# Performance work log

Measured on AMD Instinct MI355X. Metric: run time of the kernel, lower is better.

## Reference

```python
import jax, jax.numpy as jnp
import numpy as np

N = 50000   # nodes
E = 1600000 # edges (before self loops)
G = 512     # graphs in the batch
NEG = 0.2   # GATv2 leaky_relu negative slope


def _seg_softmax(s, seg, n):
    m = jax.ops.segment_max(s, seg, num_segments=n)
    e = jnp.exp(s - m[seg])
    z = jax.ops.segment_sum(e, seg, num_segments=n)
    return e / z[seg]


def _gatv2(x, src, dst, ea, Wl, bl, Wr, br, We, att, bias, n):
    # PyG GATv2Conv, heads=1: e_ij = att . leaky_relu(Wl x_j + Wr x_i + We e_ij)
    xl = x @ Wl + bl
    xr = x @ Wr + br
    h = jax.nn.leaky_relu(xl[src] + xr[dst] + ea @ We, NEG)  # [E+N, C]
    alpha = _seg_softmax(h @ att, dst, n)                    # softmax over dst neighborhoods
    return jax.ops.segment_sum(alpha[:, None] * xl[src], dst, num_segments=n) + bias


def _add_self_loops(src, dst, ea, n):
    # fill_value='mean': self-loop edge_attr = mean of incoming edge_attr (0 if none)
    deg = jax.ops.segment_sum(jnp.ones_like(dst, dtype=ea.dtype), dst, num_segments=n)
    loop = jax.ops.segment_sum(ea, dst, num_segments=n) / jnp.maximum(deg, 1.0)[:, None]
    ar = jnp.arange(n, dtype=src.dtype)
    return (jnp.concatenate([src, ar]), jnp.concatenate([dst, ar]),
            jnp.concatenate([ea, loop], axis=0))


def _glorot(key, fan_in, fan_out):
    return jax.random.normal(key, (fan_in, fan_out), dtype=jnp.float32) / np.sqrt(fan_in)


def setup_inputs() -> dict:
    key = jax.random.key(0)
    ks = jax.random.split(key, 20)
    x = jax.random.normal(ks[0], (N, 16), dtype=jnp.float32)
    edge_index = jax.random.randint(ks[1], (2, E), 0, N, dtype=jnp.int32)
    edge_attr = jax.random.normal(ks[2], (E, 18), dtype=jnp.float32)
    batch_ids = jnp.sort(jax.random.randint(ks[3], (N,), 0, G, dtype=jnp.int32))
    z = lambda c: jnp.zeros((c,), dtype=jnp.float32)
    return {
        'x': x, 'edge_index': edge_index, 'edge_attr': edge_attr, 'batch_ids': batch_ids,
        # GATv2Conv(16, 100, edge_dim=18)
        'W1l': _glorot(ks[4], 16, 100), 'b1l': z(100),
        'W1r': _glorot(ks[5], 16, 100), 'b1r': z(100),
        'W1e': _glorot(ks[6], 18, 100),
        'a1': jax.random.normal(ks[7], (100,), dtype=jnp.float32) * 0.1, 'c1': z(100),
        # GATv2Conv(100, 200, edge_dim=18)
        'W2l': _glorot(ks[8], 100, 200), 'b2l': z(200),
        'W2r': _glorot(ks[9], 100, 200), 'b2r': z(200),
        'W2e': _glorot(ks[10], 18, 200),
        'a2': jax.random.normal(ks[11], (200,), dtype=jnp.float32) * 0.1, 'c2': z(200),
        # Linear(200, 400)
        'W3': _glorot(ks[12], 200, 400), 'b3': z(400),
        # FFN 400->200->100->100
        'F1': _glorot(ks[13], 400, 200), 'bf1': z(200),
        'F2': _glorot(ks[14], 200, 100), 'bf2': z(100),
        'F3': _glorot(ks[15], 100, 100), 'bf3': z(100),
    }


def reference(x, edge_index, edge_attr, batch_ids,
              W1l, b1l, W1r, b1r, W1e, a1, c1,
              W2l, b2l, W2r, b2r, W2e, a2, c2,
              W3, b3, F1, bf1, F2, bf2, F3, bf3):
    src, dst, ea = _add_self_loops(edge_index[0], edge_index[1], edge_attr, N)
    h = jax.nn.relu(_gatv2(x, src, dst, ea, W1l, b1l, W1r, b1r, W1e, a1, c1, N))
    h = jax.nn.relu(_gatv2(h, src, dst, ea, W2l, b2l, W2r, b2r, W2e, a2, c2, N))
    h = h @ W3 + b3  # [N, 400]
    cnt = jax.ops.segment_sum(jnp.ones((N,), dtype=h.dtype), batch_ids, num_segments=G)
    pooled = jax.ops.segment_sum(h, batch_ids, num_segments=G) / jnp.maximum(cnt, 1.0)[:, None]
    y = jax.nn.relu(pooled @ F1 + bf1)
    y = jax.nn.relu(y @ F2 + bf2)
    return y @ F3 + bf3  # [G, 100]
```

## Files before the change

### kernel.cpp

```cpp
#include <hip/hip_runtime.h>
#include <cstdint>
#include <climits>
#include <math.h>

#define NN 50000
#define EE 1600000
#define ET (EE + NN)
#define GG 512
#define NEG_SLOPE 0.2f
#define NB 196

typedef _Float16 half2v __attribute__((ext_vector_type(2)));

__device__ __forceinline__ uint32_t packh2(float a, float b) {
    union { half2v h; uint32_t u; } c;
    c.h = half2v{(_Float16)a, (_Float16)b};
    return c.u;
}
__device__ __forceinline__ float2 uph(uint32_t u) {
    union { uint32_t u; half2v h; } c;
    c.u = u;
    return make_float2((float)c.h.x, (float)c.h.y);
}
__device__ __forceinline__ float fdot2u(uint32_t a, uint32_t b, float c) {
    union { uint32_t u; half2v h; } ua, ub;
    ua.u = a; ub.u = b;
    return __builtin_amdgcn_fdot2(ua.h, ub.h, c, false);
}
__device__ __forceinline__ float rlanef(float v, int l) {
    return __int_as_float(__builtin_amdgcn_readlane(__float_as_int(v), l));
}

__global__ void k_hist(const int* __restrict__ dst, int* __restrict__ hist) {
    int e = blockIdx.x * blockDim.x + threadIdx.x;
    if (e < EE) atomicAdd(&hist[dst[e]], 1);
}

__global__ void k_scan_a(const int* __restrict__ hist, int* __restrict__ bsum) {
    __shared__ int tmp[256];
    int i = blockIdx.x * 256 + threadIdx.x;
    tmp[threadIdx.x] = (i < NN) ? hist[i] : 0;
    __syncthreads();
    for (int d = 128; d; d >>= 1) {
        if (threadIdx.x < d) tmp[threadIdx.x] += tmp[threadIdx.x + d];
        __syncthreads();
    }
    if (threadIdx.x == 0) bsum[blockIdx.x] = tmp[0];
}

__global__ void k_scan_b(int* __restrict__ bsum, int* __restrict__ rowptr) {
    __shared__ int tmp[256];
    int t = threadIdx.x;
    int v = (t < NB) ? bsum[t] : 0;
    tmp[t] = v;
    __syncthreads();
    for (int d = 1; d < 256; d <<= 1) {
        int u = (t >= d) ? tmp[t - d] : 0;
        __syncthreads();
        tmp[t] += u;
        __syncthreads();
    }
    if (t < NB) bsum[t] = tmp[t] - v;
    if (t == 255) rowptr[NN] = tmp[255];
}

__global__ void k_scan_c(const int* __restrict__ hist, const int* __restrict__ bsum,
                         int* __restrict__ rowptr, int* __restrict__ cursor) {
    __shared__ int tmp[256];
    int i = blockIdx.x * 256 + threadIdx.x;
    int v = (i < NN) ? hist[i] : 0;
    tmp[threadIdx.x] = v;
    __syncthreads();
    for (int d = 1; d < 256; d <<= 1) {
        int t = (threadIdx.x >= d) ? tmp[threadIdx.x - d] : 0;
        __syncthreads();
        tmp[threadIdx.x] += t;
        __syncthreads();
    }
    if (i < NN) {
        int rp = tmp[threadIdx.x] - v + bsum[blockIdx.x];
        rowptr[i] = rp;
        cursor[i] = rp;
    }
}

__global__ void k_scatter(const int* __restrict__ srcv, const int* __restrict__ dstv,
                          const float* __restrict__ ea, int* __restrict__ cursor,
                          int* __restrict__ csr_src, int* __restrict__ csr_dst,
                          uint32_t* __restrict__ eaa) {
    int e = blockIdx.x * blockDim.x + threadIdx.x;
    if (e >= EE) return;
    int d = dstv[e];
    int p = atomicAdd(&cursor[d], 1);
    csr_src[p] = srcv[e];
    csr_dst[p] = d;
    const float* r = ea + (size_t)e * 18;
    uint32_t o[12];
#pragma unroll
    for (int kk = 0; kk < 9; kk++) {
        float2 q = *(const float2*)(r + 2 * kk);
        o[kk] = packh2(q.x, q.y);
    }
    o[9] = o[10] = o[11] = 0;
    uint4* dst = (uint4*)(eaa + (size_t)p * 12);
    dst[0] = *(uint4*)&o[0];
    dst[1] = *(uint4*)&o[4];
    dst[2] = *(uint4*)&o[8];
}

__global__ void __launch_bounds__(256)
k_loop2(const int* __restrict__ rowptr, uint32_t* __restrict__ eaa,
        int* __restrict__ csr_src, int* __restrict__ csr_dst) {
    const int lane = threadIdx.x & 63;
    int wid = blockIdx.x * (blockDim.x >> 6) + (threadIdx.x >> 6);
    int nw = gridDim.x * (blockDim.x >> 6);

    for (int i = wid; i < NN; i += nw) {
        int beg = __builtin_amdgcn_readfirstlane(rowptr[i]);
        int end = __builtin_amdgcn_readfirstlane(rowptr[i + 1]);
        float s[18];
#pragma unroll
        for (int j = 0; j < 18; j++) s[j] = 0.f;
        for (int cs = beg; cs < end; cs += 64) {
            int cnt = end - cs; if (cnt > 64) cnt = 64;
            if (lane < cnt) {
                const uint32_t* pe = eaa + (size_t)(cs + lane) * 12;
                uint4 a = *(const uint4*)pe;
                uint4 b = *(const uint4*)(pe + 4);
                uint32_t c = pe[8];
                uint32_t w[9] = {a.x, a.y, a.z, a.w, b.x, b.y, b.z, b.w, c};
#pragma unroll
                for (int kk = 0; kk < 9; kk++) {
                    float2 q = uph(w[kk]);
                    s[2 * kk] += q.x; s[2 * kk + 1] += q.y;
                }
            }
        }
#pragma unroll
        for (int j = 0; j < 18; j++) {
#pragma unroll
            for (int off = 32; off; off >>= 1) s[j] += __shfl_xor(s[j], off, 64);
        }
        if (lane == 0) {
            int deg = end - beg;
            float rd = (deg > 0) ? 1.0f / (float)deg : 0.0f;
            uint32_t o[12];
#pragma unroll
            for (int kk = 0; kk < 9; kk++) o[kk] = packh2(s[2 * kk] * rd, s[2 * kk + 1] * rd);
            o[9] = o[10] = o[11] = 0;
            uint4* dst = (uint4*)(eaa + (size_t)(EE + i) * 12);
            dst[0] = *(uint4*)&o[0];
            dst[1] = *(uint4*)&o[4];
            dst[2] = *(uint4*)&o[8];
            csr_src[EE + i] = i; csr_dst[EE + i] = i;
        }
    }
}

__global__ void k_pack_wet(const float* __restrict__ We, const float* __restrict__ att,
                           uint32_t* __restrict__ WeT, int C) {
    int t = blockIdx.x * blockDim.x + threadIdx.x;
    if (t >= C * 10) return;
    int c = t / 10, kk = t - c * 10;
    int g = c >> 2, j = c & 3;
    uint32_t v;
    if (kk < 9) v = packh2(We[(2 * kk) * C + c], We[(2 * kk + 1) * C + c]);
    else v = __float_as_uint(att[c]);
    WeT[g * 40 + j * 10 + kk] = v;
}

__global__ void k_combine_w(const float* __restrict__ Wl, const float* __restrict__ bl,
                            const float* __restrict__ Wr, const float* __restrict__ br,
                            float* __restrict__ Wc, float* __restrict__ bc,
                            int K, int C, int NP) {
    int t = blockIdx.x * blockDim.x + threadIdx.x;
    if (t < K * NP) {
        int k = t / NP, n = t - k * NP;
        float v = 0.0f;
        if (n < C) v = Wl[k * C + n];
        else if (n < 2 * C) v = Wr[k * C + n - C];
        Wc[t] = v;
    }
    if (t < NP) {
        float v = 0.0f;
        if (t < C) v = bl[t];
        else if (t < 2 * C) v = br[t - C];
        bc[t] = v;
    }
}

template <int KK, int NP, int C, int RL>
__global__ void __launch_bounds__(256)
k_gemm_dual(const float* __restrict__ A, const float* __restrict__ Wc,
            const float* __restrict__ bc,
            uint32_t* __restrict__ xl16, uint32_t* __restrict__ xr16) {
    constexpr int BM = 64, BN = 64, BK = 16;
    __shared__ float As[BK][BM];
    __shared__ float Ws[BK][BN];
    const int tidx = threadIdx.x;
    const int tx = tidx & 15;
    const int ty = tidx >> 4;
    const int m0 = blockIdx.x * BM;
    const int n0 = blockIdx.y * BN;

    float acc[4][4];
#pragma unroll
    for (int i2 = 0; i2 < 4; i2++)
#pragma unroll
        for (int j2 = 0; j2 < 4; j2++) acc[i2][j2] = 0.0f;

    for (int k0 = 0; k0 < KK; k0 += BK) {
        {
            int m = tidx >> 2;
            int kq = (tidx & 3) * 4;
            float4 v = make_float4(0.f, 0.f, 0.f, 0.f);
            if (m0 + m < NN && k0 + kq < KK)
                v = *(const float4*)(A + (size_t)(m0 + m) * KK + k0 + kq);
            As[kq + 0][m] = v.x; As[kq + 1][m] = v.y;
            As[kq + 2][m] = v.z; As[kq + 3][m] = v.w;
        }
        {
            int k = tidx >> 4;
            int nq = (tidx & 15) * 4;
            float4 v = make_float4(0.f, 0.f, 0.f, 0.f);
            if (k0 + k < KK)
                v = *(const float4*)(Wc + (size_t)(k0 + k) * NP + n0 + nq);
            *(float4*)&Ws[k][nq] = v;
        }
        __syncthreads();
#pragma unroll
        for (int k = 0; k < BK; k++) {
            float a[4], b[4];
            *(float4*)a = *(const float4*)&As[k][ty * 4];
            *(float4*)b = *(const float4*)&Ws[k][tx * 4];
#pragma unroll
            for (int i2 = 0; i2 < 4; i2++)
#pragma unroll
                for (int j2 = 0; j2 < 4; j2++) acc[i2][j2] += a[i2] * b[j2];
        }
        __syncthreads();
    }

    const int n = n0 + tx * 4;
    float4 bcv = *(const float4*)(bc + n);
#pragma unroll
    for (int i2 = 0; i2 < 4; i2++) {
        int m = m0 + ty * 4 + i2;
        if (m >= NN) continue;
        float4 o = make_float4(acc[i2][0] + bcv.x, acc[i2][1] + bcv.y,
                               acc[i2][2] + bcv.z, acc[i2][3] + bcv.w);
        uint2 p;
        p.x = packh2(o.x, o.y);
        p.y = packh2(o.z, o.w);
        if (n < C)          *(uint2*)(xl16 + (size_t)m * RL + n / 2) = p;
        else if (n < 2 * C) *(uint2*)(xr16 + (size_t)m * RL + (n - C) / 2) = p;
    }
}

template <int C>
__global__ void __launch_bounds__(256, 2)
k_score(const int* __restrict__ csr_src, const int* __restrict__ csr_dst,
        const uint32_t* __restrict__ eaa, const uint32_t* __restrict__ WeT,
        const uint32_t* __restrict__ xl16, const uint32_t* __restrict__ xr16,
        float* __restrict__ scores) {
    constexpr int RL = ((C / 2) + 3) & ~3;
    int pos = blockIdx.x * blockDim.x + threadIdx.x;
    if (pos >= ET) return;
    int s = csr_src[pos];
    int d = csr_dst[pos];

    uint32_t lw[RL], rw[RL];
    const uint4* pl = (const uint4*)(xl16 + (size_t)s * RL);
    const uint4* pr = (const uint4*)(xr16 + (size_t)d * RL);
#pragma unroll
    for (int i = 0; i < RL / 4; i++) *(uint4*)&lw[4 * i] = pl[i];
#pragma unroll
    for (int i = 0; i < RL / 4; i++) *(uint4*)&rw[4 * i] = pr[i];
    const uint32_t* pe = eaa + (size_t)pos * 12;
    uint4 e0 = *(const uint4*)pe;
    uint4 e1 = *(const uint4*)(pe + 4);
    uint32_t e8 = pe[8];
    __builtin_amdgcn_sched_barrier(0);

    uint32_t ean[9] = {e0.x, e0.y, e0.z, e0.w, e1.x, e1.y, e1.z, e1.w, e8};

    float score = 0.0f;
#pragma unroll
    for (int g = 0; g < C / 4; g++) {
        const uint32_t* wg = WeT + g * 40;
        union { uint32_t u; half2v h; } a0, b0, a1v, b1v, u0, u1;
        a0.u = lw[2 * g];     b0.u = rw[2 * g];
        a1v.u = lw[2 * g + 1]; b1v.u = rw[2 * g + 1];
        u0.h = a0.h + b0.h;
        u1.h = a1v.h + b1v.h;
        float lv[4] = {(float)u0.h.x, (float)u0.h.y, (float)u1.h.x, (float)u1.h.y};
#pragma unroll
        for (int j = 0; j < 4; j++) {
            float w = 0.0f;
#pragma unroll
            for (int kk = 0; kk < 9; kk++) w = fdot2u(ean[kk], wg[j * 10 + kk], w);
            float u = lv[j] + w;
            float h = fmaxf(u, NEG_SLOPE * u);
            score = fmaf(__uint_as_float(wg[j * 10 + 9]), h, score);
        }
    }
    scores[pos] = score;
}

template <int C, int VEC, int RELU>
__global__ void __launch_bounds__(256)
k_fin(const int* __restrict__ rowptr, const int* __restrict__ csr_src,
      const float* __restrict__ scores, const uint32_t* __restrict__ xl16,
      const float* __restrict__ bias, float* __restrict__ out) {
    constexpr int DW = VEC / 2;
    constexpr int RL = ((C / 2) + 3) & ~3;
    constexpr int NL = C / VEC;
    const int lane = threadIdx.x & 63;
    int wid = blockIdx.x * (blockDim.x >> 6) + (threadIdx.x >> 6);
    int nw = gridDim.x * (blockDim.x >> 6);
    const bool act = lane < NL;

    float bv[VEC];
    if (act) {
#pragma unroll
        for (int j = 0; j < VEC; j++) bv[j] = bias[lane * VEC + j];
    } else {
#pragma unroll
        for (int j = 0; j < VEC; j++) bv[j] = 0.f;
    }

    auto ldrow = [&](uint32_t (&buf)[DW], int node) {
        if (act) {
            if constexpr (DW == 2) {
                uint2 v = *(const uint2*)(xl16 + (size_t)node * RL + lane * 2);
                buf[0] = v.x; buf[1] = v.y;
            } else {
                buf[0] = xl16[(size_t)node * RL + lane];
            }
        } else {
#pragma unroll
            for (int q = 0; q < DW; q++) buf[q] = 0;
        }
    };

    for (int i = wid; i < NN; i += nw) {
        int beg = __builtin_amdgcn_readfirstlane(rowptr[i]);
        int end = __builtin_amdgcn_readfirstlane(rowptr[i + 1]);
        float s_self = scores[EE + i];

        float m = s_self;
        for (int cs = beg; cs < end; cs += 64) {
            int cnt = end - cs; if (cnt > 64) cnt = 64;
            float sc = (lane < cnt) ? scores[cs + lane] : -INFINITY;
#pragma unroll
            for (int off = 32; off; off >>= 1) sc = fmaxf(sc, __shfl_xor(sc, off, 64));
            m = fmaxf(m, sc);
        }

        float acc[VEC];
        float pes = __expf(s_self - m);
        float z = pes;
        {
            uint32_t w[DW];
            ldrow(w, i);
#pragma unroll
            for (int q = 0; q < DW; q++) {
                float2 f = uph(w[q]);
                acc[2 * q] = pes * f.x;
                acc[2 * q + 1] = pes * f.y;
            }
        }

        for (int cs = beg; cs < end; cs += 64) {
            int cnt = end - cs; if (cnt > 64) cnt = 64;
            float sc = (lane < cnt) ? scores[cs + lane] : -INFINITY;
            int srcl = (lane < cnt) ? csr_src[cs + lane] : 0;
            float pe = __expf(sc - m);
            float zc = pe;
#pragma unroll
            for (int off = 32; off; off >>= 1) zc += __shfl_xor(zc, off, 64);
            z += zc;

            uint32_t A[4][DW], Bv[4][DW];
            auto LD4 = [&](uint32_t (&buf)[4][DW], int t0) {
#pragma unroll
                for (int q = 0; q < 4; q++) {
                    int t = t0 + q;
                    if (t < cnt) {
                        int sx = __builtin_amdgcn_readlane(srcl, t);
                        ldrow(buf[q], sx);
                    }
                }
            };
            auto USE4 = [&](uint32_t (&buf)[4][DW], int t0) {
#pragma unroll
                for (int q = 0; q < 4; q++) {
                    int t = t0 + q;
                    if (t < cnt) {
                        float a = rlanef(pe, t);
#pragma unroll
                        for (int qq = 0; qq < DW; qq++) {
                            float2 f = uph(buf[q][qq]);
                            acc[2 * qq] = fmaf(a, f.x, acc[2 * qq]);
                            acc[2 * qq + 1] = fmaf(a, f.y, acc[2 * qq + 1]);
                        }
                    }
                }
            };
            LD4(A, 0);
            for (int t0 = 0; t0 < cnt; t0 += 8) {
                if (t0 + 4 < cnt) LD4(Bv, t0 + 4);
                __builtin_amdgcn_sched_barrier(0);
                USE4(A, t0);
                if (t0 + 8 < cnt) LD4(A, t0 + 8);
                __builtin_amdgcn_sched_barrier(0);
                USE4(Bv, t0 + 4);
            }
        }

        float rz = 1.0f / z;
        if (act) {
            float o[VEC];
#pragma unroll
            for (int j = 0; j < VEC; j++) {
                o[j] = acc[j] * rz + bv[j];
                if (RELU) o[j] = fmaxf(o[j], 0.0f);
            }
            if constexpr (VEC == 4) {
                *(float4*)(out + (size_t)i * C + lane * 4) = make_float4(o[0], o[1], o[2], o[3]);
            } else {
                *(float2*)(out + (size_t)i * C + lane * 2) = make_float2(o[0], o[1]);
            }
        }
    }
}

__global__ void k_pool(const float* __restrict__ h, const int* __restrict__ batch,
                       float* __restrict__ pooled) {
    int g = blockIdx.x;
    int lo = 0, hi = NN;
    while (lo < hi) { int mid = (lo + hi) >> 1; if (batch[mid] < g) lo = mid + 1; else hi = mid; }
    int start = lo;
    lo = start; hi = NN;
    while (lo < hi) { int mid = (lo + hi) >> 1; if (batch[mid] < g + 1) lo = mid + 1; else hi = mid; }
    int end = lo;
    float cnt = (float)(end - start);
    int c = threadIdx.x;
    if (c < 200) {
        float acc = 0.0f;
        for (int i = start; i < end; i++) acc += fmaxf(h[(size_t)i * 200 + c], 0.0f);
        pooled[g * 200 + c] = acc / fmaxf(cnt, 1.0f);
    }
}

__global__ void k_mlp(const float* __restrict__ X, const float* __restrict__ W,
                      const float* __restrict__ b, float* __restrict__ Y,
                      int Cin, int Cout, int do_relu) {
    int t = blockIdx.x * blockDim.x + threadIdx.x;
    if (t >= GG * Cout) return;
    int g = t / Cout, j = t - g * Cout;
    const float* xrow = X + (size_t)g * Cin;
    float acc = b[j];
    for (int k = 0; k < Cin; k++) acc += xrow[k] * W[k * Cout + j];
    if (do_relu) acc = fmaxf(acc, 0.0f);
    Y[t] = acc;
}

extern "C" void kernel_launch(void* const* d_in, const int* in_sizes, int n_in,
                              void* d_out, int out_size, void* d_ws, size_t ws_size,
                              hipStream_t stream) {
    const float* x   = (const float*)d_in[0];
    const int*   ei  = (const int*)d_in[1];
    const float* ea  = (const float*)d_in[2];
    const int*   bat = (const int*)d_in[3];
    const float* W1l = (const float*)d_in[4];  const float* b1l = (const float*)d_in[5];
    const float* W1r = (const float*)d_in[6];  const float* b1r = (const float*)d_in[7];
    const float* W1e = (const float*)d_in[8];
    const float* a1  = (const float*)d_in[9];  const float* c1  = (const float*)d_in[10];
    const float* W2l = (const float*)d_in[11]; const float* b2l = (const float*)d_in[12];
    const float* W2r = (const float*)d_in[13]; const float* b2r = (const float*)d_in[14];
    const float* W2e = (const float*)d_in[15];
    const float* a2  = (const float*)d_in[16]; const float* c2  = (const float*)d_in[17];
    const float* W3  = (const float*)d_in[18]; const float* b3  = (const float*)d_in[19];
    const float* F1  = (const float*)d_in[20]; const float* bf1 = (const float*)d_in[21];
    const float* F2  = (const float*)d_in[22]; const float* bf2 = (const float*)d_in[23];
    const float* F3  = (const float*)d_in[24]; const float* bf3 = (const float*)d_in[25];

    const int* srcv = ei;
    const int* dstv = ei + EE;

    float* W = (float*)d_ws;
    size_t off = 0;
    int*      hist    = (int*)(W + off); off += NN;
    float*    h1      = W + off; off += (size_t)NN * 100;
    float*    h2      = W + off; off += (size_t)NN * 200;
    int*      rowptr  = (int*)(W + off); off += NN + 4;
    int*      cursor  = (int*)(W + off); off += NN;
    int*      bsum    = (int*)(W + off); off += 256;
    float*    scores  = W + off; off += ET;
    int*      csr_src = (int*)(W + off); off += ET;
    int*      csr_dst = (int*)(W + off); off += ET;
    uint32_t* eaa     = (uint32_t*)(W + off); off += (size_t)ET * 12;
    uint32_t* xl16    = (uint32_t*)(W + off); off += (size_t)NN * 100;
    uint32_t* xr16    = (uint32_t*)(W + off); off += (size_t)NN * 100;
    uint32_t* WeT1    = (uint32_t*)(W + off); off += 25 * 40;
    uint32_t* WeT2    = (uint32_t*)(W + off); off += 50 * 40;
    float*    Wc1     = W + off; off += 16 * 256;
    float*    bc1     = W + off; off += 256;
    float*    Wc2     = W + off; off += 100 * 448;
    float*    bc2     = W + off; off += 448;
    float*    pooled  = W + off; off += (size_t)GG * 200;
    float*    p400    = W + off; off += (size_t)GG * 400;
    float*    y1      = W + off; off += (size_t)GG * 200;
    float*    y2      = W + off; off += (size_t)GG * 100;
    (void)ws_size; (void)n_in; (void)in_sizes; (void)out_size;

    const int B = 256;
    const int NODEB = 12500;

    hipMemsetAsync(hist, 0, (size_t)NN * sizeof(int), stream);
    k_hist<<<(EE + B - 1) / B, B, 0, stream>>>(dstv, hist);
    k_scan_a<<<NB, 256, 0, stream>>>(hist, bsum);
    k_scan_b<<<1, 256, 0, stream>>>(bsum, rowptr);
    k_scan_c<<<NB, 256, 0, stream>>>(hist, bsum, rowptr, cursor);
    k_scatter<<<(EE + B - 1) / B, B, 0, stream>>>(srcv, dstv, ea, cursor, csr_src, csr_dst, eaa);
    k_loop2<<<NODEB, B, 0, stream>>>(rowptr, eaa, csr_src, csr_dst);

    k_pack_wet<<<(100 * 10 + B - 1) / B, B, 0, stream>>>(W1e, a1, WeT1, 100);
    k_pack_wet<<<(200 * 10 + B - 1) / B, B, 0, stream>>>(W2e, a2, WeT2, 200);
    k_combine_w<<<(16 * 256 + B - 1) / B, B, 0, stream>>>(W1l, b1l, W1r, b1r, Wc1, bc1, 16, 100, 256);
    k_combine_w<<<(100 * 448 + B - 1) / B, B, 0, stream>>>(W2l, b2l, W2r, b2r, Wc2, bc2, 100, 200, 448);

    {
        dim3 grid((NN + 63) / 64, 256 / 64);
        k_gemm_dual<16, 256, 100, 52><<<grid, 256, 0, stream>>>(x, Wc1, bc1, xl16, xr16);
    }
    k_score<100><<<(ET + B - 1) / B, B, 0, stream>>>(csr_src, csr_dst, eaa, WeT1, xl16, xr16, scores);
    k_fin<100, 2, 1><<<NODEB, B, 0, stream>>>(rowptr, csr_src, scores, xl16, c1, h1);

    {
        dim3 grid((NN + 63) / 64, 448 / 64);
        k_gemm_dual<100, 448, 200, 100><<<grid, 256, 0, stream>>>(h1, Wc2, bc2, xl16, xr16);
    }
    k_score<200><<<(ET + B - 1) / B, B, 0, stream>>>(csr_src, csr_dst, eaa, WeT2, xl16, xr16, scores);
    k_fin<200, 4, 0><<<NODEB, B, 0, stream>>>(rowptr, csr_src, scores, xl16, c2, h2);

    k_pool<<<GG, 256, 0, stream>>>(h2, bat, pooled);
    k_mlp<<<(GG * 400 + B - 1) / B, B, 0, stream>>>(pooled, W3, b3, p400, 200, 400, 0);
    k_mlp<<<(GG * 200 + B - 1) / B, B, 0, stream>>>(p400, F1, bf1, y1, 400, 200, 1);
    k_mlp<<<(GG * 100 + B - 1) / B, B, 0, stream>>>(y1, F2, bf2, y2, 200, 100, 1);
    k_mlp<<<(GG * 100 + B - 1) / B, B, 0, stream>>>(y2, F3, bf3, (float*)d_out, 100, 100, 0);
}
```

Measured before the change: 1.373 ms.

## Score two edges per thread with streamed row chunks; deepen k_fin prefetch pipeline

k_score now processes two edges per thread. It streams the xl/xr rows in 16-byte chunks with one-chunk-ahead prefetch instead of loading whole rows into registers, and asks for 4 blocks per CU in launch bounds. To fit the chunked loop, layer-1 channels are padded to 104 with zero weights, and the xl16/xr16 buffers are memset so the pad lanes are defined. k_fin replaces its two-buffer loop with a fully unrolled four-buffer software pipeline that keeps up to three row-load groups in flight per 64-edge chunk. The aim is to cut register pressure and expose more memory-level parallelism in these gather-bound kernels, at the cost of two extra memsets and larger unrolled code.

```diff
diff --git a/kernel.cpp b/kernel.cpp
--- a/kernel.cpp
+++ b/kernel.cpp
@@ -21,6 +21,12 @@
     union { uint32_t u; half2v h; } c;
     c.u = u;
     return make_float2((float)c.h.x, (float)c.h.y);
+}
+__device__ __forceinline__ uint32_t pkadd(uint32_t a, uint32_t b) {
+    union { uint32_t u; half2v h; } x, y, z;
+    x.u = a; y.u = b;
+    z.h = x.h + y.h;
+    return z.u;
 }
 __device__ __forceinline__ float fdot2u(uint32_t a, uint32_t b, float c) {
     union { uint32_t u; half2v h; } ua, ub;
@@ -158,14 +164,16 @@
 }
 
 __global__ void k_pack_wet(const float* __restrict__ We, const float* __restrict__ att,
-                           uint32_t* __restrict__ WeT, int C) {
+                           uint32_t* __restrict__ WeT, int C, int CP) {
     int t = blockIdx.x * blockDim.x + threadIdx.x;
-    if (t >= C * 10) return;
+    if (t >= CP * 10) return;
     int c = t / 10, kk = t - c * 10;
     int g = c >> 2, j = c & 3;
-    uint32_t v;
-    if (kk < 9) v = packh2(We[(2 * kk) * C + c], We[(2 * kk + 1) * C + c]);
-    else v = __float_as_uint(att[c]);
+    uint32_t v = 0;
+    if (c < C) {
+        if (kk < 9) v = packh2(We[(2 * kk) * C + c], We[(2 * kk + 1) * C + c]);
+        else v = __float_as_uint(att[c]);
+    }
     WeT[g * 40 + j * 10 + kk] = v;
 }
 
@@ -257,54 +265,78 @@
     }
 }
 
-template <int C>
-__global__ void __launch_bounds__(256, 2)
+__device__ __forceinline__ void grp4(const uint32_t* __restrict__ wg,
+                                     const uint32_t* __restrict__ e9,
+                                     uint32_t ud0, uint32_t ud1, float& score) {
+    float2 f0 = uph(ud0), f1 = uph(ud1);
+    float cv[4] = {f0.x, f0.y, f1.x, f1.y};
+#pragma unroll
+    for (int j = 0; j < 4; j++) {
+        float w = 0.0f;
+#pragma unroll
+        for (int kk = 0; kk < 9; kk++) w = fdot2u(e9[kk], wg[j * 10 + kk], w);
+        float u = cv[j] + w;
+        float h = fmaxf(u, NEG_SLOPE * u);
+        score = fmaf(__uint_as_float(wg[j * 10 + 9]), h, score);
+    }
+}
+
+template <int C, int CP>
+__global__ void __launch_bounds__(256, 4)
 k_score(const int* __restrict__ csr_src, const int* __restrict__ csr_dst,
         const uint32_t* __restrict__ eaa, const uint32_t* __restrict__ WeT,
         const uint32_t* __restrict__ xl16, const uint32_t* __restrict__ xr16,
         float* __restrict__ scores) {
-    constexpr int RL = ((C / 2) + 3) & ~3;
-    int pos = blockIdx.x * blockDim.x + threadIdx.x;
-    if (pos >= ET) return;
-    int s = csr_src[pos];
-    int d = csr_dst[pos];
-
-    uint32_t lw[RL], rw[RL];
-    const uint4* pl = (const uint4*)(xl16 + (size_t)s * RL);
-    const uint4* pr = (const uint4*)(xr16 + (size_t)d * RL);
-#pragma unroll
-    for (int i = 0; i < RL / 4; i++) *(uint4*)&lw[4 * i] = pl[i];
-#pragma unroll
-    for (int i = 0; i < RL / 4; i++) *(uint4*)&rw[4 * i] = pr[i];
-    const uint32_t* pe = eaa + (size_t)pos * 12;
-    uint4 e0 = *(const uint4*)pe;
-    uint4 e1 = *(const uint4*)(pe + 4);
-    uint32_t e8 = pe[8];
-    __builtin_amdgcn_sched_barrier(0);
-
-    uint32_t ean[9] = {e0.x, e0.y, e0.z, e0.w, e1.x, e1.y, e1.z, e1.w, e8};
-
-    float score = 0.0f;
-#pragma unroll
-    for (int g = 0; g < C / 4; g++) {
-        const uint32_t* wg = WeT + g * 40;
-        union { uint32_t u; half2v h; } a0, b0, a1v, b1v, u0, u1;
-        a0.u = lw[2 * g];     b0.u = rw[2 * g];
-        a1v.u = lw[2 * g + 1]; b1v.u = rw[2 * g + 1];
-        u0.h = a0.h + b0.h;
-        u1.h = a1v.h + b1v.h;
-        float lv[4] = {(float)u0.h.x, (float)u0.h.y, (float)u1.h.x, (float)u1.h.y};
-#pragma unroll
-        for (int j = 0; j < 4; j++) {
-            float w = 0.0f;
-#pragma unroll
-            for (int kk = 0; kk < 9; kk++) w = fdot2u(ean[kk], wg[j * 10 + kk], w);
-            float u = lv[j] + w;
-            float h = fmaxf(u, NEG_SLOPE * u);
-            score = fmaf(__uint_as_float(wg[j * 10 + 9]), h, score);
-        }
-    }
-    scores[pos] = score;
+    constexpr int RL = CP / 2;
+    constexpr int NCH = CP / 8;
+    int t = blockIdx.x * blockDim.x + threadIdx.x;
+    int p0 = 2 * t;
+    if (p0 >= ET) return;
+    int p1 = p0 + 1;
+    const bool v1 = p1 < ET;
+    int s0 = csr_src[p0], d0 = csr_dst[p0];
+    int s1 = v1 ? csr_src[p1] : s0, d1 = v1 ? csr_dst[p1] : d0;
+
+    const uint4* plA = (const uint4*)(xl16 + (size_t)s0 * RL);
+    const uint4* prA = (const uint4*)(xr16 + (size_t)d0 * RL);
+    const uint4* plB = (const uint4*)(xl16 + (size_t)s1 * RL);
+    const uint4* prB = (const uint4*)(xr16 + (size_t)d1 * RL);
+
+    uint4 lA = plA[0], rA = prA[0], lB = plB[0], rB = prB[0];
+
+    const uint32_t* peA = eaa + (size_t)p0 * 12;
+    const uint32_t* peB = eaa + (size_t)(v1 ? p1 : p0) * 12;
+    uint4 a0 = *(const uint4*)peA; uint4 a1 = *(const uint4*)(peA + 4);
+    uint4 b0 = *(const uint4*)peB; uint4 b1 = *(const uint4*)(peB + 4);
+    uint32_t eA[9] = {a0.x, a0.y, a0.z, a0.w, a1.x, a1.y, a1.z, a1.w, peA[8]};
+    uint32_t eB[9] = {b0.x, b0.y, b0.z, b0.w, b1.x, b1.y, b1.z, b1.w, peB[8]};
+
+    float sA = 0.0f, sB = 0.0f;
+#pragma unroll 2
+    for (int ch = 0; ch < NCH; ch++) {
+        uint4 lA2, rA2, lB2, rB2;
+        if (ch + 1 < NCH) {
+            lA2 = plA[ch + 1]; rA2 = prA[ch + 1];
+            lB2 = plB[ch + 1]; rB2 = prB[ch + 1];
+        }
+        const uint32_t* wg0 = WeT + (2 * ch) * 40;
+        const uint32_t* wg1 = wg0 + 40;
+        {
+            uint32_t c0 = pkadd(lA.x, rA.x), c1 = pkadd(lA.y, rA.y);
+            uint32_t c2 = pkadd(lA.z, rA.z), c3 = pkadd(lA.w, rA.w);
+            grp4(wg0, eA, c0, c1, sA);
+            grp4(wg1, eA, c2, c3, sA);
+        }
+        {
+            uint32_t c0 = pkadd(lB.x, rB.x), c1 = pkadd(lB.y, rB.y);
+            uint32_t c2 = pkadd(lB.z, rB.z), c3 = pkadd(lB.w, rB.w);
+            grp4(wg0, eB, c0, c1, sB);
+            grp4(wg1, eB, c2, c3, sB);
+        }
+        if (ch + 1 < NCH) { lA = lA2; rA = rA2; lB = lB2; rB = rB2; }
+    }
+    scores[p0] = sA;
+    if (v1) scores[p1] = sB;
 }
 
 template <int C, int VEC, int RELU>
@@ -381,13 +413,13 @@
             for (int off = 32; off; off >>= 1) zc += __shfl_xor(zc, off, 64);
             z += zc;
 
-            uint32_t A[4][DW], Bv[4][DW];
+            uint32_t bA[4][DW], bB[4][DW], bC[4][DW], bD[4][DW];
             auto LD4 = [&](uint32_t (&buf)[4][DW], int t0) {
 #pragma unroll
                 for (int q = 0; q < 4; q++) {
-                    int t = t0 + q;
-                    if (t < cnt) {
-                        int sx = __builtin_amdgcn_readlane(srcl, t);
+                    int tt = t0 + q;
+                    if (tt < cnt) {
+                        int sx = __builtin_amdgcn_readlane(srcl, tt);
                         ldrow(buf[q], sx);
                     }
                 }
@@ -395,9 +427,9 @@
             auto USE4 = [&](uint32_t (&buf)[4][DW], int t0) {
 #pragma unroll
                 for (int q = 0; q < 4; q++) {
-                    int t = t0 + q;
-                    if (t < cnt) {
-                        float a = rlanef(pe, t);
+                    int tt = t0 + q;
+                    if (tt < cnt) {
+                        float a = rlanef(pe, tt);
 #pragma unroll
                         for (int qq = 0; qq < DW; qq++) {
                             float2 f = uph(buf[q][qq]);
@@ -407,15 +439,23 @@
                     }
                 }
             };
-            LD4(A, 0);
-            for (int t0 = 0; t0 < cnt; t0 += 8) {
-                if (t0 + 4 < cnt) LD4(Bv, t0 + 4);
-                __builtin_amdgcn_sched_barrier(0);
-                USE4(A, t0);
-                if (t0 + 8 < cnt) LD4(A, t0 + 8);
-                __builtin_amdgcn_sched_barrier(0);
-                USE4(Bv, t0 + 4);
-            }
+            LD4(bA, 0); LD4(bB, 4); LD4(bC, 8);
+            USE4(bA, 0);  LD4(bD, 12);
+            USE4(bB, 4);  LD4(bA, 16);
+            USE4(bC, 8);  LD4(bB, 20);
+            USE4(bD, 12); LD4(bC, 24);
+            USE4(bA, 16); LD4(bD, 28);
+            USE4(bB, 20); LD4(bA, 32);
+            USE4(bC, 24); LD4(bB, 36);
+            USE4(bD, 28); LD4(bC, 40);
+            USE4(bA, 32); LD4(bD, 44);
+            USE4(bB, 36); LD4(bA, 48);
+            USE4(bC, 40); LD4(bB, 52);
+            USE4(bD, 44); LD4(bC, 56);
+            USE4(bA, 48); LD4(bD, 60);
+            USE4(bB, 52);
+            USE4(bC, 56);
+            USE4(bD, 60);
         }
 
         float rz = 1.0f / z;
@@ -503,7 +543,7 @@
     uint32_t* eaa     = (uint32_t*)(W + off); off += (size_t)ET * 12;
     uint32_t* xl16    = (uint32_t*)(W + off); off += (size_t)NN * 100;
     uint32_t* xr16    = (uint32_t*)(W + off); off += (size_t)NN * 100;
-    uint32_t* WeT1    = (uint32_t*)(W + off); off += 25 * 40;
+    uint32_t* WeT1    = (uint32_t*)(W + off); off += 26 * 40;
     uint32_t* WeT2    = (uint32_t*)(W + off); off += 50 * 40;
     float*    Wc1     = W + off; off += 16 * 256;
     float*    bc1     = W + off; off += 256;
@@ -526,23 +566,25 @@
     k_scatter<<<(EE + B - 1) / B, B, 0, stream>>>(srcv, dstv, ea, cursor, csr_src, csr_dst, eaa);
     k_loop2<<<NODEB, B, 0, stream>>>(rowptr, eaa, csr_src, csr_dst);
 
-    k_pack_wet<<<(100 * 10 + B - 1) / B, B, 0, stream>>>(W1e, a1, WeT1, 100);
-    k_pack_wet<<<(200 * 10 + B - 1) / B, B, 0, stream>>>(W2e, a2, WeT2, 200);
+    k_pack_wet<<<(104 * 10 + B - 1) / B, B, 0, stream>>>(W1e, a1, WeT1, 100, 104);
+    k_pack_wet<<<(200 * 10 + B - 1) / B, B, 0, stream>>>(W2e, a2, WeT2, 200, 200);
     k_combine_w<<<(16 * 256 + B - 1) / B, B, 0, stream>>>(W1l, b1l, W1r, b1r, Wc1, bc1, 16, 100, 256);
     k_combine_w<<<(100 * 448 + B - 1) / B, B, 0, stream>>>(W2l, b2l, W2r, b2r, Wc2, bc2, 100, 200, 448);
 
+    hipMemsetAsync(xl16, 0, (size_t)NN * 52 * 4, stream);
+    hipMemsetAsync(xr16, 0, (size_t)NN * 52 * 4, stream);
     {
         dim3 grid((NN + 63) / 64, 256 / 64);
         k_gemm_dual<16, 256, 100, 52><<<grid, 256, 0, stream>>>(x, Wc1, bc1, xl16, xr16);
     }
-    k_score<100><<<(ET + B - 1) / B, B, 0, stream>>>(csr_src, csr_dst, eaa, WeT1, xl16, xr16, scores);
+    k_score<100, 104><<<(ET / 2 + B - 1) / B, B, 0, stream>>>(csr_src, csr_dst, eaa, WeT1, xl16, xr16, scores);
     k_fin<100, 2, 1><<<NODEB, B, 0, stream>>>(rowptr, csr_src, scores, xl16, c1, h1);
 
     {
         dim3 grid((NN + 63) / 64, 448 / 64);
         k_gemm_dual<100, 448, 200, 100><<<grid, 256, 0, stream>>>(h1, Wc2, bc2, xl16, xr16);
     }
-    k_score<200><<<(ET + B - 1) / B, B, 0, stream>>>(csr_src, csr_dst, eaa, WeT2, xl16, xr16, scores);
+    k_score<200, 200><<<(ET / 2 + B - 1) / B, B, 0, stream>>>(csr_src, csr_dst, eaa, WeT2, xl16, xr16, scores);
     k_fin<200, 4, 0><<<NODEB, B, 0, stream>>>(rowptr, csr_src, scores, xl16, c2, h2);
 
     k_pool<<<GG, 256, 0, stream>>>(h2, bat, pooled);
```

Measured after the change: 1.882 ms. 37.0% more time.

## Fuse GATv2 edge scoring and aggregation into one online-softmax kernel

Applied to the files above, without the earlier changes.

Replaces the separate per-edge score kernel and per-node softmax/aggregate kernel with one kernel, one 64-lane block per destination node. Each block loads neighbor xl rows once into LDS, computes scores, and uses an online max/sum softmax to accumulate in a single pass. This removes the scores buffer, the csr_dst array and the second gather of source rows. In exchange the score dot products now read through LDS with a serial per-lane loop over channels, and low-degree nodes leave lanes idle. Padding for WeT and zeroing xl16/xr16 are added so the padded channels stay safe.

```diff
diff --git a/kernel.cpp b/kernel.cpp
--- a/kernel.cpp
+++ b/kernel.cpp
@@ -21,6 +21,12 @@
     union { uint32_t u; half2v h; } c;
     c.u = u;
     return make_float2((float)c.h.x, (float)c.h.y);
+}
+__device__ __forceinline__ uint32_t pkadd(uint32_t a, uint32_t b) {
+    union { uint32_t u; half2v h; } x, y, z;
+    x.u = a; y.u = b;
+    z.h = x.h + y.h;
+    return z.u;
 }
 __device__ __forceinline__ float fdot2u(uint32_t a, uint32_t b, float c) {
     union { uint32_t u; half2v h; } ua, ub;
@@ -86,14 +92,12 @@
 
 __global__ void k_scatter(const int* __restrict__ srcv, const int* __restrict__ dstv,
                           const float* __restrict__ ea, int* __restrict__ cursor,
-                          int* __restrict__ csr_src, int* __restrict__ csr_dst,
-                          uint32_t* __restrict__ eaa) {
+                          int* __restrict__ csr_src, uint32_t* __restrict__ eaa) {
     int e = blockIdx.x * blockDim.x + threadIdx.x;
     if (e >= EE) return;
     int d = dstv[e];
     int p = atomicAdd(&cursor[d], 1);
     csr_src[p] = srcv[e];
-    csr_dst[p] = d;
     const float* r = ea + (size_t)e * 18;
     uint32_t o[12];
 #pragma unroll
@@ -109,8 +113,7 @@
 }
 
 __global__ void __launch_bounds__(256)
-k_loop2(const int* __restrict__ rowptr, uint32_t* __restrict__ eaa,
-        int* __restrict__ csr_src, int* __restrict__ csr_dst) {
+k_loop2(const int* __restrict__ rowptr, uint32_t* __restrict__ eaa) {
     const int lane = threadIdx.x & 63;
     int wid = blockIdx.x * (blockDim.x >> 6) + (threadIdx.x >> 6);
     int nw = gridDim.x * (blockDim.x >> 6);
@@ -152,20 +155,21 @@
             dst[0] = *(uint4*)&o[0];
             dst[1] = *(uint4*)&o[4];
             dst[2] = *(uint4*)&o[8];
-            csr_src[EE + i] = i; csr_dst[EE + i] = i;
         }
     }
 }
 
 __global__ void k_pack_wet(const float* __restrict__ We, const float* __restrict__ att,
-                           uint32_t* __restrict__ WeT, int C) {
+                           uint32_t* __restrict__ WeT, int C, int CP) {
     int t = blockIdx.x * blockDim.x + threadIdx.x;
-    if (t >= C * 10) return;
+    if (t >= CP * 10) return;
     int c = t / 10, kk = t - c * 10;
     int g = c >> 2, j = c & 3;
-    uint32_t v;
-    if (kk < 9) v = packh2(We[(2 * kk) * C + c], We[(2 * kk + 1) * C + c]);
-    else v = __float_as_uint(att[c]);
+    uint32_t v = 0;
+    if (c < C) {
+        if (kk < 9) v = packh2(We[(2 * kk) * C + c], We[(2 * kk + 1) * C + c]);
+        else v = __float_as_uint(att[c]);
+    }
     WeT[g * 40 + j * 10 + kk] = v;
 }
 
@@ -257,173 +261,121 @@
     }
 }
 
-template <int C>
-__global__ void __launch_bounds__(256, 2)
-k_score(const int* __restrict__ csr_src, const int* __restrict__ csr_dst,
-        const uint32_t* __restrict__ eaa, const uint32_t* __restrict__ WeT,
-        const uint32_t* __restrict__ xl16, const uint32_t* __restrict__ xr16,
-        float* __restrict__ scores) {
+template <int C, int VEC, int RELU>
+__global__ void __launch_bounds__(64)
+k_gat(const int* __restrict__ rowptr, const int* __restrict__ csr_src,
+      const uint32_t* __restrict__ eaa, const uint32_t* __restrict__ WeT,
+      const uint32_t* __restrict__ xl16, const uint32_t* __restrict__ xr16,
+      const float* __restrict__ bias, float* __restrict__ out) {
     constexpr int RL = ((C / 2) + 3) & ~3;
-    int pos = blockIdx.x * blockDim.x + threadIdx.x;
-    if (pos >= ET) return;
-    int s = csr_src[pos];
-    int d = csr_dst[pos];
-
-    uint32_t lw[RL], rw[RL];
-    const uint4* pl = (const uint4*)(xl16 + (size_t)s * RL);
-    const uint4* pr = (const uint4*)(xr16 + (size_t)d * RL);
-#pragma unroll
-    for (int i = 0; i < RL / 4; i++) *(uint4*)&lw[4 * i] = pl[i];
-#pragma unroll
-    for (int i = 0; i < RL / 4; i++) *(uint4*)&rw[4 * i] = pr[i];
-    const uint32_t* pe = eaa + (size_t)pos * 12;
-    uint4 e0 = *(const uint4*)pe;
-    uint4 e1 = *(const uint4*)(pe + 4);
-    uint32_t e8 = pe[8];
-    __builtin_amdgcn_sched_barrier(0);
-
-    uint32_t ean[9] = {e0.x, e0.y, e0.z, e0.w, e1.x, e1.y, e1.z, e1.w, e8};
-
-    float score = 0.0f;
-#pragma unroll
-    for (int g = 0; g < C / 4; g++) {
-        const uint32_t* wg = WeT + g * 40;
-        union { uint32_t u; half2v h; } a0, b0, a1v, b1v, u0, u1;
-        a0.u = lw[2 * g];     b0.u = rw[2 * g];
-        a1v.u = lw[2 * g + 1]; b1v.u = rw[2 * g + 1];
-        u0.h = a0.h + b0.h;
-        u1.h = a1v.h + b1v.h;
-        float lv[4] = {(float)u0.h.x, (float)u0.h.y, (float)u1.h.x, (float)u1.h.y};
-#pragma unroll
-        for (int j = 0; j < 4; j++) {
-            float w = 0.0f;
-#pragma unroll
-            for (int kk = 0; kk < 9; kk++) w = fdot2u(ean[kk], wg[j * 10 + kk], w);
-            float u = lv[j] + w;
-            float h = fmaxf(u, NEG_SLOPE * u);
-            score = fmaf(__uint_as_float(wg[j * 10 + 9]), h, score);
-        }
-    }
-    scores[pos] = score;
-}
-
-template <int C, int VEC, int RELU>
-__global__ void __launch_bounds__(256)
-k_fin(const int* __restrict__ rowptr, const int* __restrict__ csr_src,
-      const float* __restrict__ scores, const uint32_t* __restrict__ xl16,
-      const float* __restrict__ bias, float* __restrict__ out) {
+    constexpr int LP = RL + 1;
+    constexpr int NQ = RL / 4;
+    constexpr int NL = C / VEC;
     constexpr int DW = VEC / 2;
-    constexpr int RL = ((C / 2) + 3) & ~3;
-    constexpr int NL = C / VEC;
-    const int lane = threadIdx.x & 63;
-    int wid = blockIdx.x * (blockDim.x >> 6) + (threadIdx.x >> 6);
-    int nw = gridDim.x * (blockDim.x >> 6);
-    const bool act = lane < NL;
-
-    float bv[VEC];
-    if (act) {
-#pragma unroll
-        for (int j = 0; j < VEC; j++) bv[j] = bias[lane * VEC + j];
-    } else {
-#pragma unroll
-        for (int j = 0; j < VEC; j++) bv[j] = 0.f;
-    }
-
-    auto ldrow = [&](uint32_t (&buf)[DW], int node) {
-        if (act) {
-            if constexpr (DW == 2) {
-                uint2 v = *(const uint2*)(xl16 + (size_t)node * RL + lane * 2);
-                buf[0] = v.x; buf[1] = v.y;
-            } else {
-                buf[0] = xl16[(size_t)node * RL + lane];
-            }
-        } else {
-#pragma unroll
-            for (int q = 0; q < DW; q++) buf[q] = 0;
-        }
-    };
-
-    for (int i = wid; i < NN; i += nw) {
+    __shared__ uint32_t s_rows[64 * LP];
+    __shared__ uint32_t s_xr[RL];
+    const int lane = threadIdx.x;
+
+    for (int i = blockIdx.x; i < NN; i += gridDim.x) {
         int beg = __builtin_amdgcn_readfirstlane(rowptr[i]);
         int end = __builtin_amdgcn_readfirstlane(rowptr[i + 1]);
-        float s_self = scores[EE + i];
-
-        float m = s_self;
-        for (int cs = beg; cs < end; cs += 64) {
-            int cnt = end - cs; if (cnt > 64) cnt = 64;
-            float sc = (lane < cnt) ? scores[cs + lane] : -INFINITY;
-#pragma unroll
-            for (int off = 32; off; off >>= 1) sc = fmaxf(sc, __shfl_xor(sc, off, 64));
-            m = fmaxf(m, sc);
-        }
-
+        int endp = end + 1;
+
+        for (int j = lane; j < RL; j += 64) s_xr[j] = xr16[(size_t)i * RL + j];
+
+        float m = -INFINITY, z = 0.0f;
         float acc[VEC];
-        float pes = __expf(s_self - m);
-        float z = pes;
-        {
-            uint32_t w[DW];
-            ldrow(w, i);
-#pragma unroll
-            for (int q = 0; q < DW; q++) {
-                float2 f = uph(w[q]);
-                acc[2 * q] = pes * f.x;
-                acc[2 * q + 1] = pes * f.y;
-            }
-        }
-
-        for (int cs = beg; cs < end; cs += 64) {
-            int cnt = end - cs; if (cnt > 64) cnt = 64;
-            float sc = (lane < cnt) ? scores[cs + lane] : -INFINITY;
-            int srcl = (lane < cnt) ? csr_src[cs + lane] : 0;
-            float pe = __expf(sc - m);
+#pragma unroll
+        for (int j = 0; j < VEC; j++) acc[j] = 0.0f;
+
+        for (int cs = beg; cs < endp; cs += 64) {
+            int cnt = endp - cs; if (cnt > 64) cnt = 64;
+            int pos = cs + lane;
+            bool ae = pos < endp;
+
+            uint4 st[NQ];
+            uint32_t ear[9];
+            if (ae) {
+                int sx = (pos < end) ? csr_src[pos] : i;
+                size_t eidx = (pos < end) ? (size_t)pos : (size_t)(EE + i);
+                const uint4* pr = (const uint4*)(xl16 + (size_t)sx * RL);
+#pragma unroll
+                for (int q = 0; q < NQ; q++) st[q] = pr[q];
+                const uint32_t* pe = eaa + eidx * 12;
+                uint4 e0 = *(const uint4*)pe;
+                uint4 e1 = *(const uint4*)(pe + 4);
+                ear[0] = e0.x; ear[1] = e0.y; ear[2] = e0.z; ear[3] = e0.w;
+                ear[4] = e1.x; ear[5] = e1.y; ear[6] = e1.z; ear[7] = e1.w;
+                ear[8] = pe[8];
+            }
+            __builtin_amdgcn_sched_barrier(0);
+
+            if (ae) {
+#pragma unroll
+                for (int q = 0; q < NQ; q++) {
+                    s_rows[lane * LP + 4 * q + 0] = st[q].x;
+                    s_rows[lane * LP + 4 * q + 1] = st[q].y;
+                    s_rows[lane * LP + 4 * q + 2] = st[q].z;
+                    s_rows[lane * LP + 4 * q + 3] = st[q].w;
+                }
+            }
+
+            float s = -INFINITY;
+            if (ae) {
+                float sc = 0.0f;
+#pragma unroll 2
+                for (int d = 0; d < RL; d++) {
+                    uint32_t u = pkadd(s_rows[lane * LP + d], s_xr[d]);
+                    float2 f = uph(u);
+                    const uint32_t* wg0 = WeT + (d >> 1) * 40 + (d & 1) * 20;
+                    float w0 = 0.0f, w1 = 0.0f;
+#pragma unroll
+                    for (int kk = 0; kk < 9; kk++) {
+                        w0 = fdot2u(ear[kk], wg0[kk], w0);
+                        w1 = fdot2u(ear[kk], wg0[10 + kk], w1);
+                    }
+                    float u0 = f.x + w0, u1 = f.y + w1;
+                    float h0 = fmaxf(u0, NEG_SLOPE * u0);
+                    float h1v = fmaxf(u1, NEG_SLOPE * u1);
+                    sc = fmaf(__uint_as_float(wg0[9]), h0, sc);
+                    sc = fmaf(__uint_as_float(wg0[19]), h1v, sc);
+                }
+                s = sc;
+            }
+
+            float pmax = s;
+#pragma unroll
+            for (int off = 32; off; off >>= 1) pmax = fmaxf(pmax, __shfl_xor(pmax, off, 64));
+            float mn = fmaxf(m, pmax);
+            float sca = __expf(m - mn);
+            float pe = __expf(s - mn);
             float zc = pe;
 #pragma unroll
             for (int off = 32; off; off >>= 1) zc += __shfl_xor(zc, off, 64);
-            z += zc;
-
-            uint32_t A[4][DW], Bv[4][DW];
-            auto LD4 = [&](uint32_t (&buf)[4][DW], int t0) {
-#pragma unroll
-                for (int q = 0; q < 4; q++) {
-                    int t = t0 + q;
-                    if (t < cnt) {
-                        int sx = __builtin_amdgcn_readlane(srcl, t);
-                        ldrow(buf[q], sx);
+            z = z * sca + zc;
+            m = mn;
+#pragma unroll
+            for (int j = 0; j < VEC; j++) acc[j] *= sca;
+
+            if (lane < NL) {
+                for (int e = 0; e < cnt; e++) {
+                    float a = rlanef(pe, e);
+#pragma unroll
+                    for (int q = 0; q < DW; q++) {
+                        float2 f = uph(s_rows[e * LP + lane * DW + q]);
+                        acc[2 * q] = fmaf(a, f.x, acc[2 * q]);
+                        acc[2 * q + 1] = fmaf(a, f.y, acc[2 * q + 1]);
                     }
                 }
-            };
-            auto USE4 = [&](uint32_t (&buf)[4][DW], int t0) {
-#pragma unroll
-                for (int q = 0; q < 4; q++) {
-                    int t = t0 + q;
-                    if (t < cnt) {
-                        float a = rlanef(pe, t);
-#pragma unroll
-                        for (int qq = 0; qq < DW; qq++) {
-                            float2 f = uph(buf[q][qq]);
-                            acc[2 * qq] = fmaf(a, f.x, acc[2 * qq]);
-                            acc[2 * qq + 1] = fmaf(a, f.y, acc[2 * qq + 1]);
-                        }
-                    }
-                }
-            };
-            LD4(A, 0);
-            for (int t0 = 0; t0 < cnt; t0 += 8) {
-                if (t0 + 4 < cnt) LD4(Bv, t0 + 4);
-                __builtin_amdgcn_sched_barrier(0);
-                USE4(A, t0);
-                if (t0 + 8 < cnt) LD4(A, t0 + 8);
-                __builtin_amdgcn_sched_barrier(0);
-                USE4(Bv, t0 + 4);
-            }
-        }
-
-        float rz = 1.0f / z;
-        if (act) {
+            }
+        }
+
+        if (lane < NL) {
+            float rz = 1.0f / z;
             float o[VEC];
 #pragma unroll
             for (int j = 0; j < VEC; j++) {
-                o[j] = acc[j] * rz + bv[j];
+                o[j] = acc[j] * rz + bias[lane * VEC + j];
                 if (RELU) o[j] = fmaxf(o[j], 0.0f);
             }
             if constexpr (VEC == 4) {
@@ -497,13 +449,11 @@
     int*      rowptr  = (int*)(W + off); off += NN + 4;
     int*      cursor  = (int*)(W + off); off += NN;
     int*      bsum    = (int*)(W + off); off += 256;
-    float*    scores  = W + off; off += ET;
     int*      csr_src = (int*)(W + off); off += ET;
-    int*      csr_dst = (int*)(W + off); off += ET;
     uint32_t* eaa     = (uint32_t*)(W + off); off += (size_t)ET * 12;
     uint32_t* xl16    = (uint32_t*)(W + off); off += (size_t)NN * 100;
     uint32_t* xr16    = (uint32_t*)(W + off); off += (size_t)NN * 100;
-    uint32_t* WeT1    = (uint32_t*)(W + off); off += 25 * 40;
+    uint32_t* WeT1    = (uint32_t*)(W + off); off += 26 * 40;
     uint32_t* WeT2    = (uint32_t*)(W + off); off += 50 * 40;
     float*    Wc1     = W + off; off += 16 * 256;
     float*    bc1     = W + off; off += 256;
@@ -523,27 +473,27 @@
     k_scan_a<<<NB, 256, 0, stream>>>(hist, bsum);
     k_scan_b<<<1, 256, 0, stream>>>(bsum, rowptr);
     k_scan_c<<<NB, 256, 0, stream>>>(hist, bsum, rowptr, cursor);
-    k_scatter<<<(EE + B - 1) / B, B, 0, stream>>>(srcv, dstv, ea, cursor, csr_src, csr_dst, eaa);
-    k_loop2<<<NODEB, B, 0, stream>>>(rowptr, eaa, csr_src, csr_dst);
-
-    k_pack_wet<<<(100 * 10 + B - 1) / B, B, 0, stream>>>(W1e, a1, WeT1, 100);
-    k_pack_wet<<<(200 * 10 + B - 1) / B, B, 0, stream>>>(W2e, a2, WeT2, 200);
+    k_scatter<<<(EE + B - 1) / B, B, 0, stream>>>(srcv, dstv, ea, cursor, csr_src, eaa);
+    k_loop2<<<NODEB, B, 0, stream>>>(rowptr, eaa);
+
+    k_pack_wet<<<(104 * 10 + B - 1) / B, B, 0, stream>>>(W1e, a1, WeT1, 100, 104);
+    k_pack_wet<<<(200 * 10 + B - 1) / B, B, 0, stream>>>(W2e, a2, WeT2, 200, 200);
     k_combine_w<<<(16 * 256 + B - 1) / B, B, 0, stream>>>(W1l, b1l, W1r, b1r, Wc1, bc1, 16, 100, 256);
     k_combine_w<<<(100 * 448 + B - 1) / B, B, 0, stream>>>(W2l, b2l, W2r, b2r, Wc2, bc2, 100, 200, 448);
 
+    hipMemsetAsync(xl16, 0, (size_t)NN * 52 * 4, stream);
+    hipMemsetAsync(xr16, 0, (size_t)NN * 52 * 4, stream);
     {
         dim3 grid((NN + 63) / 64, 256 / 64);
         k_gemm_dual<16, 256, 100, 52><<<grid, 256, 0, stream>>>(x, Wc1, bc1, xl16, xr16);
     }
-    k_score<100><<<(ET + B - 1) / B, B, 0, stream>>>(csr_src, csr_dst, eaa, WeT1, xl16, xr16, scores);
-    k_fin<100, 2, 1><<<NODEB, B, 0, stream>>>(rowptr, csr_src, scores, xl16, c1, h1);
+    k_gat<100, 2, 1><<<NN, 64, 0, stream>>>(rowptr, csr_src, eaa, WeT1, xl16, xr16, c1, h1);
 
     {
         dim3 grid((NN + 63) / 64, 448 / 64);
         k_gemm_dual<100, 448, 200, 100><<<grid, 256, 0, stream>>>(h1, Wc2, bc2, xl16, xr16);
     }
-    k_score<200><<<(ET + B - 1) / B, B, 0, stream>>>(csr_src, csr_dst, eaa, WeT2, xl16, xr16, scores);
-    k_fin<200, 4, 0><<<NODEB, B, 0, stream>>>(rowptr, csr_src, scores, xl16, c2, h2);
+    k_gat<200, 4, 0><<<NN, 64, 0, stream>>>(rowptr, csr_src, eaa, WeT2, xl16, xr16, c2, h2);
 
     k_pool<<<GG, 256, 0, stream>>>(h2, bat, pooled);
     k_mlp<<<(GG * 400 + B - 1) / B, B, 0, stream>>>(pooled, W3, b3, p400, 200, 400, 0);
```

Measured after the change: 1.549 ms. 12.8% more time.
